# Kernel optimization log

Measured on AMD Instinct MI355X. Metric: run time of the kernel, lower is better.

The kernel has to match this reference:

```python
import jax, jax.numpy as jnp
import numpy as np

E = 262144      # total neighbor edges across all (sample, timestep) pairs
B = 1024        # samples with non-zero history
L = 10          # seq_len
T = B * L       # total timesteps (segments)
H = 128         # h_dim
N_ENT = 40000
N_REL = 256


def setup_inputs() -> dict:
    key = jax.random.key(0)
    ks = jax.random.split(key, 16)
    return {
        "nbr_ent": jax.random.randint(ks[0], (E,), 0, N_ENT),
        "nbr_rel": jax.random.randint(ks[1], (E,), 0, N_REL),
        "nbr_att": jax.random.uniform(ks[2], (E,), dtype=jnp.float32),
        "seg_ids": jnp.sort(jax.random.randint(ks[3], (E,), 0, T)),
        "self_att": jax.random.uniform(ks[4], (B, L), dtype=jnp.float32),
        "s_ids": jax.random.randint(ks[5], (B,), 0, N_ENT),
        "r_ids": jax.random.randint(ks[6], (B,), 0, N_REL),
        "ent_embeds": jax.random.normal(ks[7], (N_ENT, H), dtype=jnp.float32),
        "rel_embeds": jax.random.normal(ks[8], (N_REL, H), dtype=jnp.float32),
        "W1_w": jax.random.normal(ks[9], (H, 1), dtype=jnp.float32) * 0.1,
        "W1_b": jax.random.normal(ks[10], (H,), dtype=jnp.float32) * 0.1,
        "W3_w": jax.random.normal(ks[11], (H, 3 * H), dtype=jnp.float32) * 0.05,
        "W3_b": jax.random.normal(ks[12], (H,), dtype=jnp.float32) * 0.05,
        "W4_w": jax.random.normal(ks[13], (H, 2 * H), dtype=jnp.float32) * 0.05,
        "W4_b": jax.random.normal(ks[14], (H,), dtype=jnp.float32) * 0.05,
    }


def reference(nbr_ent, nbr_rel, nbr_att, seg_ids, self_att, s_ids, r_ids,
              ent_embeds, rel_embeds, W1_w, W1_b, W3_w, W3_b, W4_w, W4_b):
    # --- per-edge embeddings (the body of get_sorted_s_r_embed) ---
    # W1: scalar attribute -> h_dim, then ReLU
    e_att = jax.nn.relu(nbr_att[:, None] * W1_w[:, 0][None, :] + W1_b)   # [E, H]
    e_s = ent_embeds[nbr_ent]                                            # [E, H]
    e_r = rel_embeds[nbr_rel]                                            # [E, H]
    e = jax.nn.relu(jnp.concatenate([e_att, e_s, e_r], -1) @ W3_w.T + W3_b)      # [E, H]
    e_static = jax.nn.relu(jnp.concatenate([e_s, e_r], -1) @ W4_w.T + W4_b)      # [E, H]

    # --- sparse-mask segment mean (torch.sparse.mm with 0/1 mask / len_s) ---
    counts = jax.ops.segment_sum(jnp.ones_like(nbr_att), seg_ids, num_segments=T)
    denom = jnp.maximum(counts, 1.0)[:, None]                            # guard empty segments
    embeds_mean = jax.ops.segment_sum(e, seg_ids, num_segments=T) / denom          # [T, H]
    embeds_static_mean = jax.ops.segment_sum(e_static, seg_ids, num_segments=T) / denom

    embeds_mean = embeds_mean.reshape(B, L, H)
    embeds_static_mean = embeds_static_mean.reshape(B, L, H)

    # --- per-sample fill of padded sequence tensors ---
    self_att_emb = jax.nn.relu(self_att[..., None] * W1_w[:, 0] + W1_b)  # [B, L, H]
    self_e = jnp.broadcast_to(ent_embeds[s_ids][:, None, :], (B, L, H))  # repeat over time
    self_r = jnp.broadcast_to(rel_embeds[r_ids][:, None, :], (B, L, H))

    s_embed_seq = jnp.concatenate([self_e, self_r, embeds_static_mean], -1)   # [B, L, 3H]
    att_embed_seq = jnp.concatenate([self_att_emb, self_e, embeds_mean], -1)  # [B, L, 3H]
    # dropout omitted (eval mode); pack_padded_sequence returns padded tensors here
    return s_embed_seq, att_embed_seq
```

## Files before the change

### kernel.cpp

```cpp
#include <hip/hip_runtime.h>
#include <hip/hip_bf16.h>

#define E_EDGES 262144
#define B_SAMP  1024
#define L_SEQ   10
#define T_SEG   (B_SAMP * L_SEQ)
#define H_DIM   128
#define N_ENT_C 40000
#define N_REL_C 256

typedef __attribute__((ext_vector_type(8))) short short8;
typedef __attribute__((ext_vector_type(4))) float f32x4;

__device__ __forceinline__ float b2f(__hip_bfloat16 x) { return __bfloat162float(x); }
__device__ __forceinline__ unsigned short f2bu(float x) {
    return __bfloat16_as_ushort(__float2bfloat16(x));
}
__device__ __forceinline__ float bu2f(unsigned short u) {
    return b2f(__ushort_as_bfloat16(u));
}

__device__ __forceinline__ float loadF(const void* base, int idx, int isB16) {
    if (isB16) return b2f(((const __hip_bfloat16*)base)[idx]);
    return ((const float*)base)[idx];
}
__device__ __forceinline__ int loadI(const void* base, int idx, int is64) {
    if (is64) return (int)(((const long long*)base)[idx]);
    return ((const int*)base)[idx];
}

__device__ __forceinline__ void detect_dtypes(const void* att_raw,
                                              const void* sid_raw,
                                              int tid, int& isB, int& i64)
{
    __shared__ int cF, cI;
    if (tid == 0) { cF = 0; cI = 0; }
    __syncthreads();
    const unsigned short* pa = (const unsigned short*)att_raw;
    int c = 0;
    for (int i = tid; i < 2048; i += 256) if (pa[i] <= 0x3F80u) c++;
    if (c) atomicAdd(&cF, c);
    const int* ps = (const int*)sid_raw;
    c = 0;
    for (int i = tid; i < 512; i += 256) if (ps[2 * i + 1] == 0) c++;
    if (c) atomicAdd(&cI, c);
    __syncthreads();
    isB = (cF >= 1900) ? 1 : 0;
    i64 = (cI >= 256) ? 1 : 0;
}

__global__ void __launch_bounds__(256)
ka_prep(const void* __restrict__ W3w, const void* __restrict__ W4w,
        const void* __restrict__ W1w, const void* __restrict__ W1b,
        const void* __restrict__ W3b, const void* __restrict__ W4b,
        const void* __restrict__ seg_ids,
        const void* __restrict__ att_raw, const void* __restrict__ sid_raw,
        unsigned short* __restrict__ wctEb, unsigned short* __restrict__ wctRb,
        float2* __restrict__ ab3, int* __restrict__ starts,
        float* __restrict__ W1w_f, float* __restrict__ W1b_f,
        float* __restrict__ W3b_f, float* __restrict__ W4b_f,
        float* __restrict__ bpts, int* __restrict__ pnIn,
        int* __restrict__ flag, int* __restrict__ iflag)
{
    const int bid = blockIdx.x, tid = threadIdx.x;
    int isB, i64;
    detect_dtypes(att_raw, sid_raw, tid, isB, i64);

    if (bid < 256) {
        int gid = bid * 256 + tid;
        if (gid < 32768) {
            int n = gid >> 7, k = gid & 127;
            float v = (n < 128) ? loadF(W3w, n * 384 + 128 + k, isB)
                                : loadF(W4w, (n - 128) * 256 + k, isB);
            wctEb[gid] = f2bu(v);
        } else {
            int j = gid - 32768;
            int n = j >> 7, k = j & 127;
            float v = (n < 128) ? loadF(W3w, n * 384 + 256 + k, isB)
                                : loadF(W4w, (n - 128) * 256 + 128 + k, isB);
            wctRb[j] = f2bu(v);
        }
        return;
    }

    if (bid < 321 || bid == 362) {
        __shared__ float w1s[128], b1s[128], srt[128];
        __shared__ int nInS;
        if (tid < 128) {
            float w = loadF(W1w, tid, isB);
            float b = loadF(W1b, tid, isB);
            w1s[tid] = w; b1s[tid] = b;
        }
        __syncthreads();
        if (tid < 128) {
            float w = w1s[tid], b = b1s[tid];
            float t = 2.0f;
            if (w != 0.0f) {
                float tt = -b / w;
                if (tt > 0.0f && tt < 1.0f) t = tt;
            }
            srt[tid] = t;
        }
        __syncthreads();
        float myt = 0.0f; int rank = 0, n = 0;
        if (tid < 128) {
            myt = srt[tid];
            for (int j = 0; j < 128; ++j) {
                float v = srt[j];
                rank += (v < myt) || (v == myt && j < tid);
                n += (v < 1.5f);
            }
        }
        __syncthreads();
        if (tid < 128) srt[rank] = myt;
        if (tid == 0) nInS = n;
        __syncthreads();
        const int nIn = nInS;

        if (bid == 362) {
            if (tid < 128) {
                W1w_f[tid] = w1s[tid];
                W1b_f[tid] = b1s[tid];
                W3b_f[tid] = loadF(W3b, tid, isB);
                W4b_f[tid] = loadF(W4b, tid, isB);
                bpts[tid] = srt[tid];
            }
            if (tid == 0) { *pnIn = nIn; *flag = isB; *iflag = i64; }
            return;
        }
        const int j = (bid - 256) * 2 + (tid >> 7);
        const int h = tid & 127;
        if (j <= nIn) {
            float left  = (j == 0)   ? 0.0f : srt[j - 1];
            float right = (j == nIn) ? 1.0f : srt[j];
            float mid = 0.5f * (left + right);
            float a = 0.0f, b = 0.0f;
            for (int k = 0; k < 128; ++k) {
                if (fmaf(mid, w1s[k], b1s[k]) > 0.0f) {
                    float w3 = loadF(W3w, h * 384 + k, isB);
                    a = fmaf(w1s[k], w3, a);
                    b = fmaf(b1s[k], w3, b);
                }
            }
            ab3[j * 128 + h] = make_float2(a, b);
        }
        return;
    }

    int t = (bid - 321) * 256 + tid;
    if (t <= T_SEG) {
        int lo = 0, hi = E_EDGES;
        while (lo < hi) {
            int m = (lo + hi) >> 1;
            if (loadI(seg_ids, m, i64) < t) lo = m + 1; else hi = m;
        }
        starts[t] = lo;
    }
}

#define KB_ENT_BLOCKS (N_ENT_C / 64)
#define KB_REL_BLOCKS (N_REL_C / 64)

__global__ void __launch_bounds__(256)
kb_gemm(const void* __restrict__ ent_raw, const void* __restrict__ rel_raw,
        const int* __restrict__ flag,
        const unsigned short* __restrict__ wctEb,
        const unsigned short* __restrict__ wctRb,
        unsigned int* __restrict__ entp2, unsigned int* __restrict__ relp2)
{
    const int isB = *flag;
    const int bid = blockIdx.x, tid = threadIdx.x;

    const void* A; const unsigned short* WT; unsigned int* out; int m0;
    if (bid < KB_ENT_BLOCKS) { A = ent_raw; WT = wctEb; out = entp2; m0 = bid * 64; }
    else { A = rel_raw; WT = wctRb; out = relp2; m0 = (bid - KB_ENT_BLOCKS) * 64; }

    __shared__ unsigned short As[64][136];

    if (isB) {
        for (int v = tid; v < 1024; v += 256) {
            int e = v * 8, r = e >> 7, cc = e & 127;
            short8 x = *(const short8*)((const short*)A + m0 * 128 + e);
            *(short8*)&As[r][cc] = x;
        }
    } else {
        for (int v = tid; v < 2048; v += 256) {
            int e = v * 4, r = e >> 7, cc = e & 127;
            float4 f = *(const float4*)((const float*)A + m0 * 128 + e);
            unsigned int lo = (unsigned int)f2bu(f.x) | ((unsigned int)f2bu(f.y) << 16);
            unsigned int hi = (unsigned int)f2bu(f.z) | ((unsigned int)f2bu(f.w) << 16);
            *(uint2*)&As[r][cc] = make_uint2(lo, hi);
        }
    }
    __syncthreads();

    const int wave = tid >> 6, lane = tid & 63;
    const int quad = lane >> 4, l16 = lane & 15;

    f32x4 acc3[8], acc4[8];
    #pragma unroll
    for (int np = 0; np < 8; ++np) {
        acc3[np] = (f32x4){0.f, 0.f, 0.f, 0.f};
        acc4[np] = (f32x4){0.f, 0.f, 0.f, 0.f};
    }

    #pragma unroll
    for (int kk = 0; kk < 4; ++kk) {
        const int kb = kk * 32 + quad * 8;
        short8 av = *(const short8*)&As[wave * 16 + l16][kb];
        #pragma unroll
        for (int np = 0; np < 8; ++np) {
            const short* bp = (const short*)WT + (np * 16 + l16) * 128 + kb;
            short8 bv3 = *(const short8*)bp;
            short8 bv4 = *(const short8*)(bp + 128 * 128);
            acc3[np] = __builtin_amdgcn_mfma_f32_16x16x32_bf16(av, bv3, acc3[np], 0, 0, 0);
            acc4[np] = __builtin_amdgcn_mfma_f32_16x16x32_bf16(av, bv4, acc4[np], 0, 0, 0);
        }
    }

    #pragma unroll
    for (int np = 0; np < 8; ++np) {
        #pragma unroll
        for (int r = 0; r < 4; ++r) {
            int m = m0 + wave * 16 + quad * 4 + r;
            int h = np * 16 + l16;
            unsigned int w = (unsigned int)f2bu(acc3[np][r])
                           | ((unsigned int)f2bu(acc4[np][r]) << 16);
            out[m * 128 + h] = w;
        }
    }
}

__global__ void __launch_bounds__(128)
kc_segment(const void* __restrict__ nbr_ent, const void* __restrict__ nbr_rel,
           const void* __restrict__ att_raw,
           const int* __restrict__ starts,
           const unsigned int* __restrict__ entp2,
           const unsigned int* __restrict__ relp2,
           const float2* __restrict__ ab3,
           const float* __restrict__ bpts_g, const int* __restrict__ pnIn,
           const float* __restrict__ W3b_f, const float* __restrict__ W4b_f,
           const void* __restrict__ sat_raw,
           const void* __restrict__ s_ids, const void* __restrict__ r_ids,
           const void* __restrict__ ent_raw, const void* __restrict__ rel_raw,
           const float* __restrict__ W1w_f, const float* __restrict__ W1b_f,
           const int* __restrict__ flag, const int* __restrict__ iflag,
           float* __restrict__ outS, float* __restrict__ outA)
{
    const int t = blockIdx.x, h = threadIdx.x;
    const int isB = *flag, i64 = *iflag;
    const int s = starts[t], e = starts[t + 1];

    __shared__ float bptsS[128];
    __shared__ int entS[128], relS[128], jS[128];
    __shared__ float attS[128];
    bptsS[h] = bpts_g[h];
    const int nIn = *pnIn;

    const float b3h = W3b_f[h], b4h = W4b_f[h];
    float acc3 = 0.0f, acc4 = 0.0f;

    for (int base = s; base < e; base += 128) {
        const int n = min(128, e - base);
        __syncthreads();
        if (h < n) {
            const int i = base + h;
            entS[h] = loadI(nbr_ent, i, i64);
            relS[h] = loadI(nbr_rel, i, i64);
            float att = loadF(att_raw, i, isB);
            attS[h] = att;
            int lo = 0, hi = nIn;
            while (lo < hi) {
                int m = (lo + hi) >> 1;
                if (bptsS[m] <= att) lo = m + 1; else hi = m;
            }
            jS[h] = lo;
        }
        __syncthreads();
        for (int ii = 0; ii < n; ++ii) {
            const int ent = entS[ii], rel = relS[ii], j = jS[ii];
            const float att = attS[ii];
            unsigned int ew = entp2[ent * 128 + h];
            unsigned int rw = relp2[rel * 128 + h];
            float2 ab = ab3[j * 128 + h];
            float p3s = bu2f((unsigned short)(ew & 0xFFFFu));
            float p4s = bu2f((unsigned short)(ew >> 16));
            float p3r = bu2f((unsigned short)(rw & 0xFFFFu));
            float p4r = bu2f((unsigned short)(rw >> 16));
            float z3 = fmaf(att, ab.x, ab.y) + p3s + p3r + b3h;
            float z4 = p4s + p4r + b4h;
            acc3 += fmaxf(z3, 0.0f);
            acc4 += fmaxf(z4, 0.0f);
        }
    }

    const int cnt = e - s;
    const float inv = (cnt > 0) ? (1.0f / (float)cnt) : 1.0f;
    const int b = t / L_SEQ;
    const int sid = loadI(s_ids, b, i64);
    const int rid = loadI(r_ids, b, i64);
    const float se = loadF(ent_raw, sid * 128 + h, isB);
    const float sr = loadF(rel_raw, rid * 128 + h, isB);
    const float sa = loadF(sat_raw, t, isB);
    const float sae = fmaxf(fmaf(sa, W1w_f[h], W1b_f[h]), 0.0f);

    const size_t bs = (size_t)t * 384;
    outS[bs + h]       = se;
    outS[bs + 128 + h] = sr;
    outS[bs + 256 + h] = acc4 * inv;
    outA[bs + h]       = sae;
    outA[bs + 128 + h] = se;
    outA[bs + 256 + h] = acc3 * inv;
}

extern "C" void kernel_launch(void* const* d_in, const int* in_sizes, int n_in,
                              void* d_out, int out_size, void* d_ws, size_t ws_size,
                              hipStream_t stream)
{
    const void* nbr_ent = d_in[0];
    const void* nbr_rel = d_in[1];
    const void* nbr_att = d_in[2];
    const void* seg_ids = d_in[3];
    const void* self_att = d_in[4];
    const void* s_ids = d_in[5];
    const void* r_ids = d_in[6];
    const void* ent_embeds = d_in[7];
    const void* rel_embeds = d_in[8];
    const void* W1w = d_in[9];
    const void* W1b = d_in[10];
    const void* W3w = d_in[11];
    const void* W3b = d_in[12];
    const void* W4w = d_in[13];
    const void* W4b = d_in[14];

    char* ws = (char*)d_ws;
    size_t off = 0;
    auto alloc = [&](size_t bytes) -> void* {
        void* p = ws + off;
        off = (off + bytes + 255) & ~(size_t)255;
        return p;
    };
    int*   flag   = (int*)alloc(4);
    int*   iflag  = (int*)alloc(4);
    int*   pnIn   = (int*)alloc(4);
    float* W1w_f  = (float*)alloc(128 * 4);
    float* W1b_f  = (float*)alloc(128 * 4);
    float* W3b_f  = (float*)alloc(128 * 4);
    float* W4b_f  = (float*)alloc(128 * 4);
    float* bpts   = (float*)alloc(128 * 4);
    int*   starts = (int*)alloc((T_SEG + 1) * 4);
    unsigned short* wctEb = (unsigned short*)alloc(256 * 128 * 2);
    unsigned short* wctRb = (unsigned short*)alloc(256 * 128 * 2);
    float2* ab3   = (float2*)alloc(129 * 128 * 8);
    unsigned int* entp2 = (unsigned int*)alloc((size_t)N_ENT_C * 128 * 4);
    unsigned int* relp2 = (unsigned int*)alloc((size_t)N_REL_C * 128 * 4);

    float* outS = (float*)d_out;
    float* outA = outS + (size_t)T_SEG * 384;

    ka_prep<<<363, 256, 0, stream>>>(W3w, W4w, W1w, W1b, W3b, W4b,
                                     seg_ids, nbr_att, s_ids,
                                     wctEb, wctRb, ab3, starts,
                                     W1w_f, W1b_f, W3b_f, W4b_f,
                                     bpts, pnIn, flag, iflag);

    kb_gemm<<<KB_ENT_BLOCKS + KB_REL_BLOCKS, 256, 0, stream>>>(
        ent_embeds, rel_embeds, flag, wctEb, wctRb, entp2, relp2);

    kc_segment<<<T_SEG, 128, 0, stream>>>(
        nbr_ent, nbr_rel, nbr_att, starts, entp2, relp2, ab3, bpts, pnIn,
        W3b_f, W4b_f, self_att, s_ids, r_ids, ent_embeds, rel_embeds,
        W1w_f, W1b_f, flag, iflag, outS, outA);
}
```

Measured before the change: 189.8 us.

## Process one sample per block with split-edge accumulation and fold biases into GEMM

```diff
diff --git a/kernel.cpp b/kernel.cpp
--- a/kernel.cpp
+++ b/kernel.cpp
@@ -15,9 +15,6 @@
 __device__ __forceinline__ float b2f(__hip_bfloat16 x) { return __bfloat162float(x); }
 __device__ __forceinline__ unsigned short f2bu(float x) {
     return __bfloat16_as_ushort(__float2bfloat16(x));
-}
-__device__ __forceinline__ float bu2f(unsigned short u) {
-    return b2f(__ushort_as_bfloat16(u));
 }
 
 __device__ __forceinline__ float loadF(const void* base, int idx, int isB16) {
@@ -166,14 +163,19 @@
         const int* __restrict__ flag,
         const unsigned short* __restrict__ wctEb,
         const unsigned short* __restrict__ wctRb,
+        const float* __restrict__ W3b_f, const float* __restrict__ W4b_f,
         unsigned int* __restrict__ entp2, unsigned int* __restrict__ relp2)
 {
     const int isB = *flag;
     const int bid = blockIdx.x, tid = threadIdx.x;
 
-    const void* A; const unsigned short* WT; unsigned int* out; int m0;
-    if (bid < KB_ENT_BLOCKS) { A = ent_raw; WT = wctEb; out = entp2; m0 = bid * 64; }
-    else { A = rel_raw; WT = wctRb; out = relp2; m0 = (bid - KB_ENT_BLOCKS) * 64; }
+    const void* A; const unsigned short* WT; unsigned int* out; int m0, isRel;
+    if (bid < KB_ENT_BLOCKS) {
+        A = ent_raw; WT = wctEb; out = entp2; m0 = bid * 64; isRel = 0;
+    } else {
+        A = rel_raw; WT = wctRb; out = relp2;
+        m0 = (bid - KB_ENT_BLOCKS) * 64; isRel = 1;
+    }
 
     __shared__ unsigned short As[64][136];
 
@@ -220,97 +222,109 @@
 
     #pragma unroll
     for (int np = 0; np < 8; ++np) {
+        int h = np * 16 + l16;
+        float bias3 = isRel ? W3b_f[h] : 0.0f;
+        float bias4 = isRel ? W4b_f[h] : 0.0f;
         #pragma unroll
         for (int r = 0; r < 4; ++r) {
             int m = m0 + wave * 16 + quad * 4 + r;
-            int h = np * 16 + l16;
-            unsigned int w = (unsigned int)f2bu(acc3[np][r])
-                           | ((unsigned int)f2bu(acc4[np][r]) << 16);
+            unsigned int w = (unsigned int)f2bu(acc3[np][r] + bias3)
+                           | ((unsigned int)f2bu(acc4[np][r] + bias4) << 16);
             out[m * 128 + h] = w;
         }
     }
 }
 
-__global__ void __launch_bounds__(128)
-kc_segment(const void* __restrict__ nbr_ent, const void* __restrict__ nbr_rel,
-           const void* __restrict__ att_raw,
-           const int* __restrict__ starts,
-           const unsigned int* __restrict__ entp2,
-           const unsigned int* __restrict__ relp2,
-           const float2* __restrict__ ab3,
-           const float* __restrict__ bpts_g, const int* __restrict__ pnIn,
-           const float* __restrict__ W3b_f, const float* __restrict__ W4b_f,
-           const void* __restrict__ sat_raw,
-           const void* __restrict__ s_ids, const void* __restrict__ r_ids,
-           const void* __restrict__ ent_raw, const void* __restrict__ rel_raw,
-           const float* __restrict__ W1w_f, const float* __restrict__ W1b_f,
-           const int* __restrict__ flag, const int* __restrict__ iflag,
-           float* __restrict__ outS, float* __restrict__ outA)
-{
-    const int t = blockIdx.x, h = threadIdx.x;
+__global__ void __launch_bounds__(256)
+kc_sample(const void* __restrict__ nbr_ent, const void* __restrict__ nbr_rel,
+          const void* __restrict__ att_raw,
+          const int* __restrict__ starts,
+          const unsigned int* __restrict__ entp2,
+          const unsigned int* __restrict__ relp2,
+          const float2* __restrict__ ab3,
+          const float* __restrict__ bpts_g, const int* __restrict__ pnIn,
+          const void* __restrict__ sat_raw,
+          const void* __restrict__ s_ids, const void* __restrict__ r_ids,
+          const void* __restrict__ ent_raw, const void* __restrict__ rel_raw,
+          const float* __restrict__ W1w_f, const float* __restrict__ W1b_f,
+          const int* __restrict__ flag, const int* __restrict__ iflag,
+          float* __restrict__ outS, float* __restrict__ outA)
+{
+    const int b = blockIdx.x, tid = threadIdx.x;
+    const int h = tid & 127, cop = tid >> 7;
     const int isB = *flag, i64 = *iflag;
-    const int s = starts[t], e = starts[t + 1];
+    const int nIn = *pnIn;
 
     __shared__ float bptsS[128];
-    __shared__ int entS[128], relS[128], jS[128];
-    __shared__ float attS[128];
-    bptsS[h] = bpts_g[h];
-    const int nIn = *pnIn;
-
-    const float b3h = W3b_f[h], b4h = W4b_f[h];
-    float acc3 = 0.0f, acc4 = 0.0f;
-
-    for (int base = s; base < e; base += 128) {
-        const int n = min(128, e - base);
-        __syncthreads();
-        if (h < n) {
-            const int i = base + h;
-            entS[h] = loadI(nbr_ent, i, i64);
-            relS[h] = loadI(nbr_rel, i, i64);
-            float att = loadF(att_raw, i, isB);
-            attS[h] = att;
-            int lo = 0, hi = nIn;
-            while (lo < hi) {
-                int m = (lo + hi) >> 1;
-                if (bptsS[m] <= att) lo = m + 1; else hi = m;
-            }
-            jS[h] = lo;
-        }
-        __syncthreads();
-        for (int ii = 0; ii < n; ++ii) {
-            const int ent = entS[ii], rel = relS[ii], j = jS[ii];
-            const float att = attS[ii];
-            unsigned int ew = entp2[ent * 128 + h];
-            unsigned int rw = relp2[rel * 128 + h];
-            float2 ab = ab3[j * 128 + h];
-            float p3s = bu2f((unsigned short)(ew & 0xFFFFu));
-            float p4s = bu2f((unsigned short)(ew >> 16));
-            float p3r = bu2f((unsigned short)(rw & 0xFFFFu));
-            float p4r = bu2f((unsigned short)(rw >> 16));
-            float z3 = fmaf(att, ab.x, ab.y) + p3s + p3r + b3h;
-            float z4 = p4s + p4r + b4h;
-            acc3 += fmaxf(z3, 0.0f);
-            acc4 += fmaxf(z4, 0.0f);
-        }
-    }
-
-    const int cnt = e - s;
-    const float inv = (cnt > 0) ? (1.0f / (float)cnt) : 1.0f;
-    const int b = t / L_SEQ;
-    const int sid = loadI(s_ids, b, i64);
-    const int rid = loadI(r_ids, b, i64);
-    const float se = loadF(ent_raw, sid * 128 + h, isB);
-    const float sr = loadF(rel_raw, rid * 128 + h, isB);
-    const float sa = loadF(sat_raw, t, isB);
-    const float sae = fmaxf(fmaf(sa, W1w_f[h], W1b_f[h]), 0.0f);
-
-    const size_t bs = (size_t)t * 384;
-    outS[bs + h]       = se;
-    outS[bs + 128 + h] = sr;
-    outS[bs + 256 + h] = acc4 * inv;
-    outA[bs + h]       = sae;
-    outA[bs + 128 + h] = se;
-    outA[bs + 256 + h] = acc3 * inv;
+    __shared__ int4 eS[256];
+    __shared__ float accS[2][128];
+
+    if (tid < 128) bptsS[tid] = bpts_g[tid];
+
+    float se = 0.f, sr = 0.f, w1 = 0.f, b1 = 0.f;
+    if (cop == 0) {
+        const int sid = loadI(s_ids, b, i64);
+        const int rid = loadI(r_ids, b, i64);
+        se = loadF(ent_raw, sid * 128 + h, isB);
+        sr = loadF(rel_raw, rid * 128 + h, isB);
+        w1 = W1w_f[h]; b1 = W1b_f[h];
+    }
+
+    for (int l = 0; l < L_SEQ; ++l) {
+        const int t = b * L_SEQ + l;
+        const int s = starts[t], e = starts[t + 1];
+        float acc3 = 0.0f, acc4 = 0.0f;
+
+        for (int base = s; base < e; base += 256) {
+            const int n = min(256, e - base);
+            __syncthreads();
+            if (tid < n) {
+                const int i = base + tid;
+                int ent = loadI(nbr_ent, i, i64);
+                int rel = loadI(nbr_rel, i, i64);
+                float att = loadF(att_raw, i, isB);
+                int lo = 0, hi = nIn;
+                while (lo < hi) {
+                    int m = (lo + hi) >> 1;
+                    if (bptsS[m] <= att) lo = m + 1; else hi = m;
+                }
+                eS[tid] = make_int4(ent, rel, __float_as_int(att), lo);
+            }
+            __syncthreads();
+            for (int ii = cop; ii < n; ii += 2) {
+                int4 q = eS[ii];
+                float att = __int_as_float(q.z);
+                unsigned int ew = entp2[q.x * 128 + h];
+                unsigned int rw = relp2[q.y * 128 + h];
+                float2 ab = ab3[q.w * 128 + h];
+                float p3s = __int_as_float(ew << 16);
+                float p4s = __int_as_float(ew & 0xFFFF0000u);
+                float p3r = __int_as_float(rw << 16);
+                float p4r = __int_as_float(rw & 0xFFFF0000u);
+                acc3 += fmaxf(fmaf(att, ab.x, ab.y) + p3s + p3r, 0.0f);
+                acc4 += fmaxf(p4s + p4r, 0.0f);
+            }
+        }
+
+        if (cop == 1) { accS[0][h] = acc3; accS[1][h] = acc4; }
+        __syncthreads();
+        if (cop == 0) {
+            acc3 += accS[0][h];
+            acc4 += accS[1][h];
+            const int cnt = e - s;
+            const float inv = (cnt > 0) ? (1.0f / (float)cnt) : 1.0f;
+            const float sa = loadF(sat_raw, t, isB);
+            const float sae = fmaxf(fmaf(sa, w1, b1), 0.0f);
+            const size_t bs = (size_t)t * 384;
+            outS[bs + h]       = se;
+            outS[bs + 128 + h] = sr;
+            outS[bs + 256 + h] = acc4 * inv;
+            outA[bs + h]       = sae;
+            outA[bs + 128 + h] = se;
+            outA[bs + 256 + h] = acc3 * inv;
+        }
+        __syncthreads();
+    }
 }
 
 extern "C" void kernel_launch(void* const* d_in, const int* in_sizes, int n_in,
@@ -365,10 +379,10 @@
                                      bpts, pnIn, flag, iflag);
 
     kb_gemm<<<KB_ENT_BLOCKS + KB_REL_BLOCKS, 256, 0, stream>>>(
-        ent_embeds, rel_embeds, flag, wctEb, wctRb, entp2, relp2);
-
-    kc_segment<<<T_SEG, 128, 0, stream>>>(
+        ent_embeds, rel_embeds, flag, wctEb, wctRb, W3b_f, W4b_f, entp2, relp2);
+
+    kc_sample<<<B_SAMP, 256, 0, stream>>>(
         nbr_ent, nbr_rel, nbr_att, starts, entp2, relp2, ab3, bpts, pnIn,
-        W3b_f, W4b_f, self_att, s_ids, r_ids, ent_embeds, rel_embeds,
+        self_att, s_ids, r_ids, ent_embeds, rel_embeds,
         W1w_f, W1b_f, flag, iflag, outS, outA);
 }
```

Result: slower. 222.5 us (+17.2%).
